# Kernel optimization log

Hardware: AMD Instinct MI355X
Metric: run time of the kernel (lower is better)

## Reference

```python
import jax, jax.numpy as jnp
from jax import lax
import numpy as np

EPS_BN = 1e-5


def _bn(x, g, b, axis):
    # eval-mode BatchNorm with running_mean=0, running_var=1
    shape = [1] * x.ndim
    shape[axis] = -1
    scale = (g / jnp.sqrt(1.0 + EPS_BN)).reshape(shape)
    return x * scale + b.reshape(shape)


def farthest_point_sample(xyz, npoint):
    B, N, _ = xyz.shape
    bidx = jnp.arange(B)

    def body(carry, _):
        dist, far = carry                      # [B,N], [B]
        centroid = xyz[bidx, far]              # [B,3]
        d = jnp.sum((xyz - centroid[:, None, :]) ** 2, axis=-1)
        dist = jnp.minimum(dist, d)
        return (dist, jnp.argmax(dist, axis=-1)), far

    init = (jnp.full((B, N), 1e10, xyz.dtype), jnp.zeros((B,), jnp.int32))
    _, idxs = lax.scan(body, init, None, length=npoint)
    return idxs.T                              # [B,npoint]


def square_distance(src, dst):
    # [B,S,3] x [B,N,3] -> [B,S,N]
    d = -2.0 * jnp.einsum('bsc,bnc->bsn', src, dst)
    d = d + jnp.sum(src ** 2, -1)[:, :, None] + jnp.sum(dst ** 2, -1)[:, None, :]
    return d


def sample_and_group(npoint, nsample, xyz, points):
    B = xyz.shape[0]
    bidx = jnp.arange(B)
    fps_idx = farthest_point_sample(xyz, npoint)          # [B,S]
    new_xyz = xyz[bidx[:, None], fps_idx]                 # [B,S,3]
    new_points = points[bidx[:, None], fps_idx]           # [B,S,C]
    dists = square_distance(new_xyz, xyz)                 # [B,S,N]
    _, idx = lax.top_k(-dists, nsample)                   # nearest nsample
    grouped = points[bidx[:, None, None], idx]            # [B,S,K,C]
    grouped_norm = grouped - new_points[:, :, None, :]
    rep = jnp.broadcast_to(new_points[:, :, None, :], grouped.shape)
    return new_xyz, jnp.concatenate([grouped_norm, rep], axis=-1)  # [B,S,K,2C]


def local_op(x, w, g, b):
    # x [B,S,K,D]; conv1d k=1 over channels D, BN, ReLU, max over K -> [B,out,S]
    y = jnp.einsum('bskd,od->bsko', x, w)
    y = jax.nn.relu(_bn(y, g, b, axis=3))
    y = jnp.max(y, axis=2)                                # [B,S,out]
    return jnp.transpose(y, (0, 2, 1))                    # [B,out,S]


def sa_layer(x, qk_w, v_w, v_b, t_w, t_b, g, b):
    # x [B,C,N]; q and k share weights (offset attention)
    xq = jnp.einsum('bcn,oc->bno', x, qk_w)               # [B,N,C/4]
    xk = jnp.einsum('bcn,oc->bon', x, qk_w)               # [B,C/4,N]
    xv = jnp.einsum('bcn,oc->bon', x, v_w) + v_b[:, None]
    energy = jnp.einsum('bnd,bdm->bnm', xq, xk)           # [B,N,N]
    attn = jax.nn.softmax(energy, axis=-1)
    attn = attn / (1e-9 + attn.sum(axis=1, keepdims=True))
    x_r = jnp.einsum('bcn,bnm->bcm', xv, attn)
    x_r = jnp.einsum('bcn,oc->bon', x - x_r, t_w) + t_b[:, None]
    x_r = jax.nn.relu(_bn(x_r, g, b, axis=1))
    return x + x_r


def setup_inputs() -> dict:
    key = jax.random.key(0)
    ks = iter(jax.random.split(key, 48))
    rn = lambda shape, s=0.05: jax.random.normal(next(ks), shape, jnp.float32) * s
    inp = {
        'xyz': jax.random.normal(next(ks), (32, 16384, 3), jnp.float32),
        'f': jax.random.normal(next(ks), (32, 16384, 3), jnp.float32),
        'conv1_w': rn((64, 6)), 'bn1_g': jnp.ones(64), 'bn1_b': jnp.zeros(64),
        'l0_w': rn((64, 128)), 'l0_g': jnp.ones(64), 'l0_b': jnp.zeros(64),
        'l1_w': rn((64, 128)), 'l1_g': jnp.ones(64), 'l1_b': jnp.zeros(64),
        'st_c1_w': rn((64, 64)), 'st_bn1_g': jnp.ones(64), 'st_bn1_b': jnp.zeros(64),
        'st_c2_w': rn((64, 64)), 'st_bn2_g': jnp.ones(64), 'st_bn2_b': jnp.zeros(64),
        'sa1_qk_w': rn((16, 64)), 'sa1_v_w': rn((64, 64)), 'sa1_v_b': jnp.zeros(64),
        'sa1_t_w': rn((64, 64)), 'sa1_t_b': jnp.zeros(64), 'sa1_g': jnp.ones(64), 'sa1_b': jnp.zeros(64),
        'sa2_qk_w': rn((16, 64)), 'sa2_v_w': rn((64, 64)), 'sa2_v_b': jnp.zeros(64),
        'sa2_t_w': rn((64, 64)), 'sa2_t_b': jnp.zeros(64), 'sa2_g': jnp.ones(64), 'sa2_b': jnp.zeros(64),
        'fuse_w': rn((256, 192)), 'fuse_g': jnp.ones(256), 'fuse_b': jnp.zeros(256),
        'lin1_w': rn((256, 256)), 'bn6_g': jnp.ones(256), 'bn6_b': jnp.zeros(256),
        'lin2_w': rn((256, 256)), 'lin2_b': jnp.zeros(256),
    }
    return inp


def _forward(xyz, f, conv1_w, bn1_g, bn1_b, l0_w, l0_g, l0_b, l1_w, l1_g, l1_b,
             st_c1_w, st_bn1_g, st_bn1_b, st_c2_w, st_bn2_g, st_bn2_b,
             sa1_qk_w, sa1_v_w, sa1_v_b, sa1_t_w, sa1_t_b, sa1_g, sa1_b,
             sa2_qk_w, sa2_v_w, sa2_v_b, sa2_t_w, sa2_t_b, sa2_g, sa2_b,
             fuse_w, fuse_g, fuse_b, lin1_w, bn6_g, bn6_b, lin2_w, lin2_b):
    center = jnp.mean(xyz, axis=1)                        # [B,3]
    xyz_c = xyz - center[:, None, :]
    pts = jnp.concatenate([xyz_c, f], axis=2)             # [B,N,6]
    geo = pts[..., :3]
    xin = jnp.transpose(pts, (0, 2, 1))                   # [B,6,N]
    x = jax.nn.relu(_bn(jnp.einsum('bcn,oc->bon', xin, conv1_w), bn1_g, bn1_b, 1))
    x = jnp.transpose(x, (0, 2, 1))                       # [B,N,64]
    new_xyz, nf = sample_and_group(128, 32, geo, x)
    feature_0 = local_op(nf, l0_w, l0_g, l0_b)            # [B,64,128]
    feature = jnp.transpose(feature_0, (0, 2, 1))
    _, nf2 = sample_and_group(32, 16, new_xyz, feature)
    feature_1 = local_op(nf2, l1_w, l1_g, l1_b)           # [B,64,32]
    # StackedAttention
    x = jax.nn.relu(_bn(jnp.einsum('bcn,oc->bon', feature_1, st_c1_w), st_bn1_g, st_bn1_b, 1))
    x = jax.nn.relu(_bn(jnp.einsum('bcn,oc->bon', x, st_c2_w), st_bn2_g, st_bn2_b, 1))
    x1 = sa_layer(x, sa1_qk_w, sa1_v_w, sa1_v_b, sa1_t_w, sa1_t_b, sa1_g, sa1_b)
    x2 = sa_layer(x1, sa2_qk_w, sa2_v_w, sa2_v_b, sa2_t_w, sa2_t_b, sa2_g, sa2_b)
    x = jnp.concatenate([x1, x2], axis=1)                 # [B,128,32]
    x = jnp.concatenate([x, feature_1], axis=1)           # [B,192,32]
    x = jax.nn.leaky_relu(_bn(jnp.einsum('bcn,oc->bon', x, fuse_w), fuse_g, fuse_b, 1), 0.2)
    x = jnp.max(x, axis=2)                                # [B,256]
    x = jax.nn.relu(_bn(x @ lin1_w.T, bn6_g, bn6_b, 1))   # dropout = identity (eval)
    x = x @ lin2_w.T + lin2_b
    return center, x


def reference(xyz, f, conv1_w, bn1_g, bn1_b, l0_w, l0_g, l0_b, l1_w, l1_g, l1_b,
              st_c1_w, st_bn1_g, st_bn1_b, st_c2_w, st_bn2_g, st_bn2_b,
              sa1_qk_w, sa1_v_w, sa1_v_b, sa1_t_w, sa1_t_b, sa1_g, sa1_b,
              sa2_qk_w, sa2_v_w, sa2_v_b, sa2_t_w, sa2_t_b, sa2_g, sa2_b,
              fuse_w, fuse_g, fuse_b, lin1_w, bn6_g, bn6_b, lin2_w, lin2_b):
    return _forward(xyz, f, conv1_w, bn1_g, bn1_b, l0_w, l0_g, l0_b, l1_w, l1_g, l1_b,
                    st_c1_w, st_bn1_g, st_bn1_b, st_c2_w, st_bn2_g, st_bn2_b,
                    sa1_qk_w, sa1_v_w, sa1_v_b, sa1_t_w, sa1_t_b, sa1_g, sa1_b,
                    sa2_qk_w, sa2_v_w, sa2_v_b, sa2_t_w, sa2_t_b, sa2_g, sa2_b,
                    fuse_w, fuse_g, fuse_b, lin1_w, bn6_g, bn6_b, lin2_w, lin2_b)
```

## Files before the change

kernel.cpp:

```cpp
#include <hip/hip_runtime.h>


__device__ __forceinline__ float bnscale(float g){ return g / sqrtf(1.0f + 1e-5f); }

__device__ __forceinline__ float conv_feat6(float p0,float p1,float p2,float p3,float p4,float p5,
                                            float w0,float w1,float w2,float w3,float w4,float w5,
                                            float sc,float bs){
    float y = p0*w0;
    y = fmaf(p1,w1,y); y = fmaf(p2,w2,y); y = fmaf(p3,w3,y);
    y = fmaf(p4,w4,y); y = fmaf(p5,w5,y);
    return fmaxf(fmaf(y,sc,bs), 0.0f);
}

__device__ __forceinline__ float fpsdist(float dx,float dy,float dz){
    #pragma clang fp contract(off)
    return (dx*dx + dy*dy) + dz*dz;
}

__device__ __forceinline__ float sumsq3(float x,float y,float z){
    #pragma clang fp contract(off)
    return (x*x + y*y) + z*z;
}
__device__ __forceinline__ float sqdist3(float qx,float qy,float qz,float qs,
                                         float px,float py,float pz){
    #pragma clang fp contract(off)
    {
        float dot = (qx*px + qy*py) + qz*pz;
        float pn  = (px*px + py*py) + pz*pz;
        return (-2.0f*dot + qs) + pn;
    }
}

__device__ __forceinline__ unsigned long long packdi(float d, unsigned int idx){
    unsigned int u = __float_as_uint(d);
    unsigned int msk = (unsigned int)((int)u >> 31);
    u ^= (msk | 0x80000000u);
    return ((unsigned long long)u << 32) | (unsigned long long)idx;
}

__device__ __forceinline__ unsigned long long u64min(unsigned long long a, unsigned long long b){
    return a < b ? a : b;
}

__device__ __forceinline__ unsigned long long u64_shfl_down(unsigned long long v, int off){
    unsigned int lo = (unsigned int)v, hi = (unsigned int)(v >> 32);
    lo = __shfl_down(lo, off, 64);
    hi = __shfl_down(hi, off, 64);
    return ((unsigned long long)hi << 32) | (unsigned long long)lo;
}

__device__ __forceinline__ unsigned long long u64_bcast0(unsigned long long v){
    unsigned int lo = (unsigned int)v, hi = (unsigned int)(v >> 32);
    lo = __shfl(lo, 0, 64);
    hi = __shfl(hi, 0, 64);
    return ((unsigned long long)hi << 32) | (unsigned long long)lo;
}

__global__ __launch_bounds__(1024, 1) void k_fps1(const float* __restrict__ xyz,
                                                  float* __restrict__ center,
                                                  float* __restrict__ out,
                                                  int* __restrict__ idx_out){
    constexpr int NTH = 1024, PPT = 16, N = 16384, NPOINT = 128, NW = 16;
    int b = blockIdx.x, t = threadIdx.x;
    int wid = t>>6, lane = t&63;

    __shared__ float s_red[NW][3];
    __shared__ unsigned int s_khi[2][NW], s_klo[2][NW];

    const float* xb = xyz + (size_t)b*N*3;
    float px[PPT], py[PPT], pz[PPT], dist[PPT];
    #pragma unroll
    for (int i=0;i<PPT;i++){
        const float* sp = xb + (size_t)(t + i*NTH)*3;
        px[i]=sp[0]; py[i]=sp[1]; pz[i]=sp[2];
        dist[i]=1e10f;
    }
    float sx=0.f, sy=0.f, sz=0.f;
    #pragma unroll
    for (int i=0;i<PPT;i++){ sx+=px[i]; sy+=py[i]; sz+=pz[i]; }
    #pragma unroll
    for (int off=32; off>=1; off>>=1){
        sx += __shfl_down(sx, off, 64);
        sy += __shfl_down(sy, off, 64);
        sz += __shfl_down(sz, off, 64);
    }
    if (lane==0){ s_red[wid][0]=sx; s_red[wid][1]=sy; s_red[wid][2]=sz; }
    __syncthreads();
    float cx0=0.f, cy0=0.f, cz0=0.f;
    #pragma unroll
    for (int w2=0; w2<NW; ++w2){ cx0+=s_red[w2][0]; cy0+=s_red[w2][1]; cz0+=s_red[w2][2]; }
    cx0 *= (1.0f/16384.0f); cy0 *= (1.0f/16384.0f); cz0 *= (1.0f/16384.0f);
    if (t < 3){
        float c = (t==0)?cx0:((t==1)?cy0:cz0);
        center[b*3+t] = c;
        out[b*3+t] = c;
    }
    #pragma unroll
    for (int i=0;i<PPT;i++){ px[i]-=cx0; py[i]-=cy0; pz[i]-=cz0; }
    if (t==0) idx_out[b*NPOINT] = 0;

    float cx = xb[0]-cx0, cy = xb[1]-cy0, cz = xb[2]-cz0;

    for (int it=1; it<NPOINT; ++it){
        int par = it & 1;
        float bv = -1.0f; int bis = 0;
        #pragma unroll
        for (int i=0;i<PPT;i++){
            float d = fpsdist(px[i]-cx, py[i]-cy, pz[i]-cz);
            float nd = fminf(dist[i], d);
            dist[i] = nd;
            bool better = nd > bv;
            bv  = better ? nd : bv;
            bis = better ? i  : bis;
        }
        int bi = t + (bis<<10);
        unsigned long long key = ((unsigned long long)__float_as_uint(bv) << 32)
                               | (unsigned long long)(unsigned)(~(unsigned)bi);
        #pragma unroll
        for (int off=32; off>=1; off>>=1){
            unsigned long long ok = u64_shfl_down(key, off);
            key = ok > key ? ok : key;
        }
        if (lane==0){ s_khi[par][wid]=(unsigned)(key>>32); s_klo[par][wid]=(unsigned)key; }
        __syncthreads();
        unsigned long long gk = ((unsigned long long)s_khi[par][0] << 32) | s_klo[par][0];
        #pragma unroll
        for (int w2=1; w2<NW; ++w2){
            unsigned long long k2 = ((unsigned long long)s_khi[par][w2] << 32) | s_klo[par][w2];
            if (k2 > gk) gk = k2;
        }
        int gi = (int)(~(unsigned)(gk & 0xFFFFFFFFull));
        gi = __builtin_amdgcn_readfirstlane(gi);
        if (t==0) idx_out[b*NPOINT + it] = gi;
        const float* wp = xb + (size_t)gi*3;
        cx = wp[0]-cx0; cy = wp[1]-cy0; cz = wp[2]-cz0;
    }
}

__global__ __launch_bounds__(256) void k_knn1(const float* __restrict__ xyz,
                                              const float* __restrict__ f,
                                              const float* __restrict__ center,
                                              const float* __restrict__ conv1_w,
                                              const float* __restrict__ bn1_g,
                                              const float* __restrict__ bn1_b,
                                              const int* __restrict__ fps_idx,
                                              float* __restrict__ new_xyz,
                                              float* __restrict__ np_feat,
                                              int* __restrict__ knn_idx){
    int t = threadIdx.x, wid = t>>6, lane = t&63;
    int q = blockIdx.x*4 + wid;
    int b = q>>7, s = q&127;

    float cx = center[b*3+0], cy = center[b*3+1], cz = center[b*3+2];
    int idx = fps_idx[b*128+s];
    const float* xp = xyz + ((size_t)b*16384 + idx)*3;
    const float* fp = f   + ((size_t)b*16384 + idx)*3;
    float p0 = xp[0]-cx, p1 = xp[1]-cy, p2 = xp[2]-cz;
    float p3 = fp[0], p4 = fp[1], p5 = fp[2];

    {
        const float* w6 = conv1_w + lane*6;
        float v = conv_feat6(p0,p1,p2,p3,p4,p5, w6[0],w6[1],w6[2],w6[3],w6[4],w6[5],
                             bnscale(bn1_g[lane]), bn1_b[lane]);
        np_feat[(size_t)q*64 + lane] = v;
        if (lane < 3){
            float pc = (lane==0)?p0:((lane==1)?p1:p2);
            new_xyz[(size_t)q*3 + lane] = pc;
        }
    }

    float qx = p0, qy = p1, qz = p2;
    float qs = sumsq3(qx,qy,qz);
    const float* xb = xyz + (size_t)b*16384*3;

    unsigned long long m0=~0ull, m1=~0ull, m2=~0ull, m3=~0ull;
    for (int i=0; i<256; i+=4){
        #pragma unroll
        for (int j=0;j<4;j++){
            int n = lane + ((i+j)<<6);
            const float* p = xb + (size_t)n*3;
            float dx = p[0]-cx, dy = p[1]-cy, dz = p[2]-cz;
            float d = sqdist3(qx,qy,qz,qs,dx,dy,dz);
            unsigned long long pk = packdi(d,(unsigned)n);
            if (j==0) m0 = u64min(m0,pk);
            else if (j==1) m1 = u64min(m1,pk);
            else if (j==2) m2 = u64min(m2,pk);
            else m3 = u64min(m3,pk);
        }
    }

    size_t kbase = (size_t)q*32;
    for (int r=0; r<32; ++r){
        unsigned long long mm = u64min(u64min(m0,m1), u64min(m2,m3));
        #pragma unroll
        for (int off=32; off>=1; off>>=1) mm = u64min(mm, u64_shfl_down(mm, off));
        unsigned long long win = u64_bcast0(mm);
        unsigned int widx = (unsigned int)(win & 0xFFFFFFFFull);
        if (lane==0) knn_idx[kbase + r] = (int)widx;
        int c = (int)(widx & 255u);
        int n2 = c + (lane<<8);
        const float* p = xb + (size_t)n2*3;
        float dx = p[0]-cx, dy = p[1]-cy, dz = p[2]-cz;
        float d = sqdist3(qx,qy,qz,qs,dx,dy,dz);
        unsigned long long pk = packdi(d,(unsigned)n2);
        if (pk <= win) pk = ~0ull;
        #pragma unroll
        for (int off=32; off>=1; off>>=1) pk = u64min(pk, u64_shfl_down(pk, off));
        unsigned long long nm = u64_bcast0(pk);
        int owner = c & 63, slot = c >> 6;
        if (lane == owner){
            if (slot==0) m0 = nm;
            else if (slot==1) m1 = nm;
            else if (slot==2) m2 = nm;
            else m3 = nm;
        }
    }
}

template<int K, int NQ, int NSRC, bool RECOMP>
__global__ __launch_bounds__(256, 2) void k_group_local(
    const float* __restrict__ xyz, const float* __restrict__ f, const float* __restrict__ center,
    const float* __restrict__ conv1_w, const float* __restrict__ bn1_g, const float* __restrict__ bn1_b,
    const float* __restrict__ src_feat,
    const int* __restrict__ knn_idx, const float* __restrict__ np_feat,
    const float* __restrict__ w, const float* __restrict__ g, const float* __restrict__ bb,
    float* __restrict__ out)
{
    __shared__ float wt[128*65];
    __shared__ float s_sc[64], s_bs[64];
    __shared__ float cwT[6*64];
    __shared__ float s_csc[64], s_cbs[64];
    __shared__ float np_l[4][64];
    __shared__ float gda[4][K][64];
    __shared__ float s_pts[4][K][6];

    int t = threadIdx.x;
    for (int e=t; e<8192; e+=256){ int o = e>>7, d = e&127; wt[d*65 + o] = w[e]; }
    if (t < 64){ s_sc[t] = bnscale(g[t]); s_bs[t] = bb[t]; }
    if constexpr (RECOMP){
        for (int e=t; e<384; e+=256){ int o = e/6, j = e%6; cwT[j*64 + o] = conv1_w[e]; }
        if (t < 64){ s_csc[t] = bnscale(bn1_g[t]); s_cbs[t] = bn1_b[t]; }
    }
    __syncthreads();

    int wid = t>>6, lane = t&63;
    int q = blockIdx.x*4 + wid;
    int b = q / NQ, s = q % NQ;

    float np_o = np_feat[((size_t)b*NQ + s)*64 + lane];
    np_l[wid][lane] = np_o;

    const int* kix = knn_idx + ((size_t)b*NQ + s)*K;

    if constexpr (RECOMP){
        float cx = center[b*3+0], cy = center[b*3+1], cz = center[b*3+2];
        if (lane < K){
            int myi = kix[lane];
            const float* xp = xyz + ((size_t)b*16384 + myi)*3;
            s_pts[wid][lane][0] = xp[0]-cx;
            s_pts[wid][lane][1] = xp[1]-cy;
            s_pts[wid][lane][2] = xp[2]-cz;
            const float* fp = f + ((size_t)b*16384 + myi)*3;
            s_pts[wid][lane][3] = fp[0];
            s_pts[wid][lane][4] = fp[1];
            s_pts[wid][lane][5] = fp[2];
        }
        #pragma unroll
        for (int k=0; k<K; ++k){
            float gv = conv_feat6(s_pts[wid][k][0], s_pts[wid][k][1], s_pts[wid][k][2],
                                  s_pts[wid][k][3], s_pts[wid][k][4], s_pts[wid][k][5],
                                  cwT[0*64+lane], cwT[1*64+lane], cwT[2*64+lane],
                                  cwT[3*64+lane], cwT[4*64+lane], cwT[5*64+lane],
                                  s_csc[lane], s_cbs[lane]);
            gda[wid][k][lane] = gv - np_o;
        }
    } else {
        int myi = kix[lane < K ? lane : 0];
        #pragma unroll
        for (int k=0; k<K; ++k){
            int ik = __shfl(myi, k, 64);
            gda[wid][k][lane] = src_feat[((size_t)b*NSRC + ik)*64 + lane] - np_o;
        }
    }

    float C = 0.f;
    #pragma unroll
    for (int d=0; d<64; d++) C = fmaf(np_l[wid][d], wt[(64+d)*65 + lane], C);

    float acc_y[K];
    #pragma unroll
    for (int k=0;k<K;k++) acc_y[k] = C;

    #pragma unroll
    for (int c=0; c<2; ++c){
        float wr[32];
        #pragma unroll
        for (int j=0;j<32;j++) wr[j] = wt[(c*32+j)*65 + lane];
        #pragma unroll
        for (int k=0;k<K;k++){
            const float4* g4 = (const float4*)&gda[wid][k][c*32];
            float yk = 0.f;
            #pragma unroll
            for (int j4=0;j4<8;j4++){
                float4 gg = g4[j4];
                yk = fmaf(gg.x, wr[j4*4+0], yk);
                yk = fmaf(gg.y, wr[j4*4+1], yk);
                yk = fmaf(gg.z, wr[j4*4+2], yk);
                yk = fmaf(gg.w, wr[j4*4+3], yk);
            }
            acc_y[k] = acc_y[k] + yk;
        }
    }

    float acc = -1e30f;
    #pragma unroll
    for (int k=0;k<K;k++){
        float v = fmaxf(fmaf(acc_y[k], s_sc[lane], s_bs[lane]), 0.0f);
        acc = fmaxf(acc, v);
    }
    out[((size_t)b*NQ + s)*64 + lane] = acc;
}

__device__ void sa_block(const float* X, float* Xout,
                         float* Q, float* E, float* XV, float* XR, float* CS,
                         const float* qk_w, const float* v_w, const float* v_b,
                         const float* t_w, const float* t_b,
                         const float* g, const float* bb, int t)
{
    constexpr int NT = 1024;
    for (int e=t; e<512; e+=NT){
        int n = e>>4, o = e&15;
        float y = 0.f;
        for (int c=0;c<64;c++) y = fmaf(qk_w[o*64+c], X[c*32+n], y);
        Q[n*16+o] = y;
    }
    for (int e=t; e<2048; e+=NT){
        int o = e>>5, n = e&31;
        float y = v_b[o];
        for (int c=0;c<64;c++) y = fmaf(v_w[o*64+c], X[c*32+n], y);
        XV[o*32+n] = y;
    }
    __syncthreads();
    {
        int n = t>>5, m = t&31;
        float y = 0.f;
        for (int d=0;d<16;d++) y = fmaf(Q[n*16+d], Q[m*16+d], y);
        E[t] = y;
    }
    __syncthreads();
    {
        float v = E[t];
        float mx = v;
        #pragma unroll
        for (int mk=16; mk>=1; mk>>=1) mx = fmaxf(mx, __shfl_xor(mx, mk, 64));
        float p = expf(v - mx);
        float sum = p;
        #pragma unroll
        for (int mk=16; mk>=1; mk>>=1) sum += __shfl_xor(sum, mk, 64);
        E[t] = p / sum;
    }
    __syncthreads();
    if (t < 32){
        float cs = 0.f;
        for (int n=0;n<32;n++) cs += E[n*32+t];
        CS[t] = 1e-9f + cs;
    }
    __syncthreads();
    E[t] = E[t] / CS[t&31];
    __syncthreads();
    for (int e=t; e<2048; e+=NT){
        int c = e>>5, m = e&31;
        float y = 0.f;
        for (int n=0;n<32;n++) y = fmaf(XV[c*32+n], E[n*32+m], y);
        XR[c*32+m] = y;
    }
    __syncthreads();
    for (int e=t; e<2048; e+=NT){
        int o = e>>5, n = e&31;
        float y = 0.f;
        for (int c=0;c<64;c++) y = fmaf(t_w[o*64+c], X[c*32+n]-XR[c*32+n], y);
        y += t_b[o];
        y = fmaxf(fmaf(y, bnscale(g[o]), bb[o]), 0.0f);
        Xout[e] = X[e] + y;
    }
    __syncthreads();
}

__global__ __launch_bounds__(1024) void k_mega(
    const float* __restrict__ new_xyz1,
    const float* __restrict__ feat,
    const float* __restrict__ l1_w, const float* __restrict__ l1_g, const float* __restrict__ l1_b,
    const float* st_c1_w, const float* st_bn1_g, const float* st_bn1_b,
    const float* st_c2_w, const float* st_bn2_g, const float* st_bn2_b,
    const float* sa1_qk, const float* sa1_v, const float* sa1_vb,
    const float* sa1_t, const float* sa1_tb, const float* sa1_g, const float* sa1_b,
    const float* sa2_qk, const float* sa2_v, const float* sa2_vb,
    const float* sa2_t, const float* sa2_tb, const float* sa2_g, const float* sa2_b,
    const float* fuse_w, const float* fuse_g, const float* fuse_b,
    const float* lin1_w, const float* bn6_g, const float* bn6_b,
    const float* lin2_w, const float* lin2_b,
    float* __restrict__ out)
{
    constexpr int NT = 1024;
    __shared__ float nx1[384];
    __shared__ int   s_i2[32];
    __shared__ float np2L[2048];
    __shared__ float nx2[96];
    __shared__ int   s_k2[512];
    __shared__ float wt[8320];
    __shared__ float s_sc[64], s_bs[64];
    __shared__ float smt[15168];

    int b = blockIdx.x, t = threadIdx.x, wid = t>>6, lane = t&63;

    for (int e=t; e<384; e+=NT) nx1[e] = new_xyz1[(size_t)b*384 + e];
    for (int e=t; e<8192; e+=NT){ int o = e>>7, d = e&127; wt[d*65 + o] = l1_w[e]; }
    if (t < 64){ s_sc[t] = bnscale(l1_g[t]); s_bs[t] = l1_b[t]; }
    __syncthreads();

    if (wid == 0){
        float px[2],py[2],pz[2],dist[2];
        #pragma unroll
        for (int i=0;i<2;i++){
            int n = lane + i*64;
            px[i]=nx1[n*3+0]; py[i]=nx1[n*3+1]; pz[i]=nx1[n*3+2];
            dist[i]=1e10f;
        }
        if (lane==0) s_i2[0] = 0;
        float cx=nx1[0], cy=nx1[1], cz=nx1[2];
        for (int it=1; it<32; ++it){
            float bv=-1.0f; int bi=0;
            float bx=0.f, by=0.f, bz=0.f;
            #pragma unroll
            for (int i=0;i<2;i++){
                float d = fpsdist(px[i]-cx, py[i]-cy, pz[i]-cz);
                float nd = fminf(dist[i], d);
                dist[i]=nd;
                bool better = nd > bv;
                bv = better ? nd : bv;
                bi = better ? (lane + i*64) : bi;
                bx = better ? px[i] : bx;
                by = better ? py[i] : by;
                bz = better ? pz[i] : bz;
            }
            unsigned long long key = ((unsigned long long)__float_as_uint(bv) << 32)
                                   | (unsigned long long)(unsigned)(~(unsigned)bi);
            #pragma unroll
            for (int off=32; off>=1; off>>=1){
                unsigned long long ok = u64_shfl_down(key, off);
                float ox = __shfl_down(bx, off, 64);
                float oy = __shfl_down(by, off, 64);
                float oz = __shfl_down(bz, off, 64);
                bool better = ok > key;
                key = better ? ok : key;
                bx = better ? ox : bx;
                by = better ? oy : by;
                bz = better ? oz : bz;
            }
            key = u64_bcast0(key);
            cx = __shfl(bx, 0, 64); cy = __shfl(by, 0, 64); cz = __shfl(bz, 0, 64);
            if (lane==0) s_i2[it] = (int)(~(unsigned)(key & 0xFFFFFFFFull));
        }
    }
    __syncthreads();

    for (int e=t; e<2048; e+=NT){
        int s = e>>6, o = e&63;
        np2L[s*64 + o] = feat[((size_t)b*128 + s_i2[s])*64 + o];
    }
    if (t < 32){
        int idx = s_i2[t];
        nx2[t*3+0] = nx1[idx*3+0];
        nx2[t*3+1] = nx1[idx*3+1];
        nx2[t*3+2] = nx1[idx*3+2];
    }
    __syncthreads();

    for (int j=0;j<2;j++){
        int s = wid + 16*j;
        float qx = nx2[s*3+0], qy = nx2[s*3+1], qz = nx2[s*3+2];
        float qs = sumsq3(qx,qy,qz);
        unsigned long long pp0, pp1;
        {
            float ax=nx1[lane*3+0], ay=nx1[lane*3+1], az=nx1[lane*3+2];
            pp0 = packdi(sqdist3(qx,qy,qz,qs,ax,ay,az), (unsigned)lane);
            ax=nx1[(lane+64)*3+0]; ay=nx1[(lane+64)*3+1]; az=nx1[(lane+64)*3+2];
            pp1 = packdi(sqdist3(qx,qy,qz,qs,ax,ay,az), (unsigned)(lane+64));
        }
        for (int r=0; r<16; ++r){
            unsigned long long mm = u64min(pp0, pp1);
            #pragma unroll
            for (int off=32; off>=1; off>>=1) mm = u64min(mm, u64_shfl_down(mm, off));
            unsigned long long win = u64_bcast0(mm);
            if (lane==0) s_k2[s*16 + r] = (int)(win & 0xFFFFFFFFull);
            if (pp0 == win) pp0 = ~0ull;
            if (pp1 == win) pp1 = ~0ull;
        }
    }
    __syncthreads();

    float* gda = smt + 2112;
    for (int j=0;j<2;j++){
        int s = wid + 16*j;
        float np_o = np2L[s*64 + lane];
        float C0 = 0.f;
        #pragma unroll
        for (int d=0; d<64; d++) C0 = fmaf(np2L[s*64 + d], wt[(64+d)*65 + lane], C0);
        float acc_y[16];
        #pragma unroll
        for (int k=0;k<16;k++) acc_y[k] = C0;
        #pragma unroll
        for (int half=0; half<2; ++half){
            #pragma unroll
            for (int kk=0;kk<8;++kk){
                int ik = s_k2[s*16 + half*8 + kk];
                gda[(wid*8+kk)*64 + lane] = feat[((size_t)b*128 + ik)*64 + lane] - np_o;
            }
            #pragma unroll
            for (int c=0; c<2; ++c){
                float wr[32];
                #pragma unroll
                for (int jj=0;jj<32;jj++) wr[jj] = wt[(c*32+jj)*65 + lane];
                #pragma unroll
                for (int kk=0;kk<8;++kk){
                    const float4* g4 = (const float4*)&gda[(wid*8+kk)*64 + c*32];
                    float yk = 0.f;
                    #pragma unroll
                    for (int j4=0;j4<8;j4++){
                        float4 gg = g4[j4];
                        yk = fmaf(gg.x, wr[j4*4+0], yk);
                        yk = fmaf(gg.y, wr[j4*4+1], yk);
                        yk = fmaf(gg.z, wr[j4*4+2], yk);
                        yk = fmaf(gg.w, wr[j4*4+3], yk);
                    }
                    acc_y[half*8+kk] = acc_y[half*8+kk] + yk;
                }
            }
        }
        float acc = -1e30f;
        #pragma unroll
        for (int k=0;k<16;k++){
            float v = fmaxf(fmaf(acc_y[k], s_sc[lane], s_bs[lane]), 0.0f);
            acc = fmaxf(acc, v);
        }
        smt[lane*33 + s] = acc;
    }
    __syncthreads();

    float* F1 = smt;
    float* XA = smt + 2112;
    float* XB = smt + 4160;
    float* Q  = smt + 6208;
    float* E  = smt + 6720;
    float* XV = smt + 7744;
    float* XR = smt + 9792;
    float* CS = smt + 11840;
    float* FO = smt + 6208;
    float* PO = smt + 14656;
    float* P2 = smt + 14912;

    for (int e=t; e<2048; e+=NT){
        int o = e>>5, n = e&31;
        float y = 0.f;
        for (int c=0;c<64;c++) y = fmaf(st_c1_w[o*64+c], F1[c*33+n], y);
        XA[e] = fmaxf(fmaf(y, bnscale(st_bn1_g[o]), st_bn1_b[o]), 0.0f);
    }
    __syncthreads();
    for (int e=t; e<2048; e+=NT){
        int o = e>>5, n = e&31;
        float y = 0.f;
        for (int c=0;c<64;c++) y = fmaf(st_c2_w[o*64+c], XA[c*32+n], y);
        XB[e] = fmaxf(fmaf(y, bnscale(st_bn2_g[o]), st_bn2_b[o]), 0.0f);
    }
    __syncthreads();
    sa_block(XB, XA, Q,E,XV,XR,CS, sa1_qk, sa1_v, sa1_vb, sa1_t, sa1_tb, sa1_g, sa1_b, t);
    sa_block(XA, XB, Q,E,XV,XR,CS, sa2_qk, sa2_v, sa2_vb, sa2_t, sa2_tb, sa2_g, sa2_b, t);
    for (int e=t; e<8192; e+=NT){
        int o = e>>5, n = e&31;
        const float* wr = fuse_w + o*192;
        float y = 0.f;
        for (int c=0;c<64;c++) y = fmaf(wr[c],      XA[c*32+n], y);
        for (int c=0;c<64;c++) y = fmaf(wr[64+c],   XB[c*32+n], y);
        for (int c=0;c<64;c++) y = fmaf(wr[128+c],  F1[c*33+n], y);
        float v = fmaf(y, bnscale(fuse_g[o]), fuse_b[o]);
        FO[o*33+n] = (v > 0.0f) ? v : 0.2f*v;
    }
    __syncthreads();
    if (t < 256){
        float mx = -1e30f;
        for (int n=0;n<32;n++) mx = fmaxf(mx, FO[t*33+n]);
        PO[t] = mx;
    }
    __syncthreads();
    if (t < 256){
        const float* wr = lin1_w + t*256;
        float y = 0.f;
        for (int c=0;c<256;c++) y = fmaf(wr[c], PO[c], y);
        P2[t] = fmaxf(fmaf(y, bnscale(bn6_g[t]), bn6_b[t]), 0.0f);
    }
    __syncthreads();
    if (t < 256){
        const float* wr = lin2_w + t*256;
        float y = 0.f;
        for (int c=0;c<256;c++) y = fmaf(wr[c], P2[c], y);
        out[96 + b*256 + t] = y + lin2_b[t];
    }
}

extern "C" void kernel_launch(void* const* d_in, const int* in_sizes, int n_in,
                              void* d_out, int out_size, void* d_ws, size_t ws_size,
                              hipStream_t stream)
{
    const float* xyz      = (const float*)d_in[0];
    const float* f        = (const float*)d_in[1];
    const float* conv1_w  = (const float*)d_in[2];
    const float* bn1_g    = (const float*)d_in[3];
    const float* bn1_b    = (const float*)d_in[4];
    const float* l0_w     = (const float*)d_in[5];
    const float* l0_g     = (const float*)d_in[6];
    const float* l0_b     = (const float*)d_in[7];
    const float* l1_w     = (const float*)d_in[8];
    const float* l1_g     = (const float*)d_in[9];
    const float* l1_b     = (const float*)d_in[10];
    const float* st_c1_w  = (const float*)d_in[11];
    const float* st_bn1_g = (const float*)d_in[12];
    const float* st_bn1_b = (const float*)d_in[13];
    const float* st_c2_w  = (const float*)d_in[14];
    const float* st_bn2_g = (const float*)d_in[15];
    const float* st_bn2_b = (const float*)d_in[16];
    const float* sa1_qk   = (const float*)d_in[17];
    const float* sa1_v    = (const float*)d_in[18];
    const float* sa1_vb   = (const float*)d_in[19];
    const float* sa1_t    = (const float*)d_in[20];
    const float* sa1_tb   = (const float*)d_in[21];
    const float* sa1_g    = (const float*)d_in[22];
    const float* sa1_b    = (const float*)d_in[23];
    const float* sa2_qk   = (const float*)d_in[24];
    const float* sa2_v    = (const float*)d_in[25];
    const float* sa2_vb   = (const float*)d_in[26];
    const float* sa2_t    = (const float*)d_in[27];
    const float* sa2_tb   = (const float*)d_in[28];
    const float* sa2_g    = (const float*)d_in[29];
    const float* sa2_b    = (const float*)d_in[30];
    const float* fuse_w   = (const float*)d_in[31];
    const float* fuse_g   = (const float*)d_in[32];
    const float* fuse_b   = (const float*)d_in[33];
    const float* lin1_w   = (const float*)d_in[34];
    const float* bn6_g    = (const float*)d_in[35];
    const float* bn6_b    = (const float*)d_in[36];
    const float* lin2_w   = (const float*)d_in[37];
    const float* lin2_b   = (const float*)d_in[38];
    float* out = (float*)d_out;

    float* ws = (float*)d_ws;
    float* center   = ws + 0;
    float* new_xyz1 = ws + 96;
    float* np1      = ws + 12384;
    float* feat     = ws + 274528;
    int*   fps1     = (int*)(ws + 536672);
    int*   knn1     = (int*)(ws + 540768);

    k_fps1<<<32, 1024, 0, stream>>>(xyz, center, out, fps1);
    k_knn1<<<1024, 256, 0, stream>>>(xyz, f, center, conv1_w, bn1_g, bn1_b,
                                     fps1, new_xyz1, np1, knn1);
    k_group_local<32,128,1,true><<<1024, 256, 0, stream>>>(
        xyz, f, center, conv1_w, bn1_g, bn1_b, nullptr, knn1, np1, l0_w, l0_g, l0_b, feat);
    k_mega<<<32, 1024, 0, stream>>>(new_xyz1, feat,
        l1_w, l1_g, l1_b,
        st_c1_w, st_bn1_g, st_bn1_b, st_c2_w, st_bn2_g, st_bn2_b,
        sa1_qk, sa1_v, sa1_vb, sa1_t, sa1_tb, sa1_g, sa1_b,
        sa2_qk, sa2_v, sa2_vb, sa2_t, sa2_tb, sa2_g, sa2_b,
        fuse_w, fuse_g, fuse_b, lin1_w, bn6_g, bn6_b, lin2_w, lin2_b, out);
}
```

Measured before the change: 724.3 us.

## Precompute centered float4 xyz with norms; stream FPS points from memory, halve block size

FPS now writes centered xyz plus squared norm as a float4 array to workspace. Each FPS iteration re-reads its points from that array instead of holding them in registers, and the block shrinks to 512 threads with 32 points per thread. The kNN and grouping kernels read the precomputed float4 points and norms, which removes the center subtraction and norm recompute, and the mega kernel is resized to 512 threads. The intent is vectorized loads and shared preprocessing, at the cost of FPS re-reading global or cache memory on every one of its 128 iterations with half the thread parallelism.

```diff
diff --git a/kernel.cpp b/kernel.cpp
--- a/kernel.cpp
+++ b/kernel.cpp
@@ -30,6 +30,14 @@
         return (-2.0f*dot + qs) + pn;
     }
 }
+__device__ __forceinline__ float sqdist3_pn(float qx,float qy,float qz,float qs,
+                                            float px,float py,float pz,float pn){
+    #pragma clang fp contract(off)
+    {
+        float dot = (qx*px + qy*py) + qz*pz;
+        return (-2.0f*dot + qs) + pn;
+    }
+}
 
 __device__ __forceinline__ unsigned long long packdi(float d, unsigned int idx){
     unsigned int u = __float_as_uint(d);
@@ -56,11 +64,11 @@
     return ((unsigned long long)hi << 32) | (unsigned long long)lo;
 }
 
-__global__ __launch_bounds__(1024, 1) void k_fps1(const float* __restrict__ xyz,
-                                                  float* __restrict__ center,
-                                                  float* __restrict__ out,
-                                                  int* __restrict__ idx_out){
-    constexpr int NTH = 1024, PPT = 16, N = 16384, NPOINT = 128, NW = 16;
+__global__ __launch_bounds__(512, 1) void k_fps1(const float* __restrict__ xyz,
+                                                 float4* xyzc,
+                                                 float* __restrict__ out,
+                                                 int* __restrict__ idx_out){
+    constexpr int NTH = 512, PPT = 32, N = 16384, NPOINT = 128, NW = 8;
     int b = blockIdx.x, t = threadIdx.x;
     int wid = t>>6, lane = t&63;
 
@@ -68,16 +76,13 @@
     __shared__ unsigned int s_khi[2][NW], s_klo[2][NW];
 
     const float* xb = xyz + (size_t)b*N*3;
-    float px[PPT], py[PPT], pz[PPT], dist[PPT];
-    #pragma unroll
+    float4* xc = xyzc + (size_t)b*N;
+
+    float sx=0.f, sy=0.f, sz=0.f;
     for (int i=0;i<PPT;i++){
         const float* sp = xb + (size_t)(t + i*NTH)*3;
-        px[i]=sp[0]; py[i]=sp[1]; pz[i]=sp[2];
-        dist[i]=1e10f;
-    }
-    float sx=0.f, sy=0.f, sz=0.f;
-    #pragma unroll
-    for (int i=0;i<PPT;i++){ sx+=px[i]; sy+=py[i]; sz+=pz[i]; }
+        sx += sp[0]; sy += sp[1]; sz += sp[2];
+    }
     #pragma unroll
     for (int off=32; off>=1; off>>=1){
         sx += __shfl_down(sx, off, 64);
@@ -92,28 +97,39 @@
     cx0 *= (1.0f/16384.0f); cy0 *= (1.0f/16384.0f); cz0 *= (1.0f/16384.0f);
     if (t < 3){
         float c = (t==0)?cx0:((t==1)?cy0:cz0);
-        center[b*3+t] = c;
         out[b*3+t] = c;
     }
-    #pragma unroll
-    for (int i=0;i<PPT;i++){ px[i]-=cx0; py[i]-=cy0; pz[i]-=cz0; }
+
+    for (int i=0;i<PPT;i++){
+        int n = t + i*NTH;
+        const float* sp = xb + (size_t)n*3;
+        float ax = sp[0]-cx0, ay = sp[1]-cy0, az = sp[2]-cz0;
+        xc[n] = make_float4(ax, ay, az, sumsq3(ax,ay,az));
+    }
     if (t==0) idx_out[b*NPOINT] = 0;
 
+    float dist[PPT];
+    #pragma unroll
+    for (int i=0;i<PPT;i++) dist[i]=1e10f;
+
     float cx = xb[0]-cx0, cy = xb[1]-cy0, cz = xb[2]-cz0;
+    __syncthreads();
 
     for (int it=1; it<NPOINT; ++it){
+        asm volatile("" ::: "memory");
         int par = it & 1;
         float bv = -1.0f; int bis = 0;
         #pragma unroll
         for (int i=0;i<PPT;i++){
-            float d = fpsdist(px[i]-cx, py[i]-cy, pz[i]-cz);
+            float4 p = xc[t + i*NTH];
+            float d = fpsdist(p.x-cx, p.y-cy, p.z-cz);
             float nd = fminf(dist[i], d);
             dist[i] = nd;
             bool better = nd > bv;
             bv  = better ? nd : bv;
             bis = better ? i  : bis;
         }
-        int bi = t + (bis<<10);
+        int bi = t + (bis<<9);
         unsigned long long key = ((unsigned long long)__float_as_uint(bv) << 32)
                                | (unsigned long long)(unsigned)(~(unsigned)bi);
         #pragma unroll
@@ -137,9 +153,8 @@
     }
 }
 
-__global__ __launch_bounds__(256) void k_knn1(const float* __restrict__ xyz,
+__global__ __launch_bounds__(256) void k_knn1(const float4* __restrict__ xyzc,
                                               const float* __restrict__ f,
-                                              const float* __restrict__ center,
                                               const float* __restrict__ conv1_w,
                                               const float* __restrict__ bn1_g,
                                               const float* __restrict__ bn1_b,
@@ -151,11 +166,11 @@
     int q = blockIdx.x*4 + wid;
     int b = q>>7, s = q&127;
 
-    float cx = center[b*3+0], cy = center[b*3+1], cz = center[b*3+2];
     int idx = fps_idx[b*128+s];
-    const float* xp = xyz + ((size_t)b*16384 + idx)*3;
-    const float* fp = f   + ((size_t)b*16384 + idx)*3;
-    float p0 = xp[0]-cx, p1 = xp[1]-cy, p2 = xp[2]-cz;
+    const float4* xcb = xyzc + (size_t)b*16384;
+    float4 qc = xcb[idx];
+    float p0 = qc.x, p1 = qc.y, p2 = qc.z;
+    const float* fp = f + ((size_t)b*16384 + idx)*3;
     float p3 = fp[0], p4 = fp[1], p5 = fp[2];
 
     {
@@ -170,17 +185,15 @@
     }
 
     float qx = p0, qy = p1, qz = p2;
-    float qs = sumsq3(qx,qy,qz);
-    const float* xb = xyz + (size_t)b*16384*3;
+    float qs = qc.w;
 
     unsigned long long m0=~0ull, m1=~0ull, m2=~0ull, m3=~0ull;
     for (int i=0; i<256; i+=4){
         #pragma unroll
         for (int j=0;j<4;j++){
             int n = lane + ((i+j)<<6);
-            const float* p = xb + (size_t)n*3;
-            float dx = p[0]-cx, dy = p[1]-cy, dz = p[2]-cz;
-            float d = sqdist3(qx,qy,qz,qs,dx,dy,dz);
+            float4 pc = xcb[n];
+            float d = sqdist3_pn(qx,qy,qz,qs, pc.x,pc.y,pc.z, pc.w);
             unsigned long long pk = packdi(d,(unsigned)n);
             if (j==0) m0 = u64min(m0,pk);
             else if (j==1) m1 = u64min(m1,pk);
@@ -199,9 +212,8 @@
         if (lane==0) knn_idx[kbase + r] = (int)widx;
         int c = (int)(widx & 255u);
         int n2 = c + (lane<<8);
-        const float* p = xb + (size_t)n2*3;
-        float dx = p[0]-cx, dy = p[1]-cy, dz = p[2]-cz;
-        float d = sqdist3(qx,qy,qz,qs,dx,dy,dz);
+        float4 pc = xcb[n2];
+        float d = sqdist3_pn(qx,qy,qz,qs, pc.x,pc.y,pc.z, pc.w);
         unsigned long long pk = packdi(d,(unsigned)n2);
         if (pk <= win) pk = ~0ull;
         #pragma unroll
@@ -217,11 +229,10 @@
     }
 }
 
-template<int K, int NQ, int NSRC, bool RECOMP>
+template<int K, int NQ>
 __global__ __launch_bounds__(256, 2) void k_group_local(
-    const float* __restrict__ xyz, const float* __restrict__ f, const float* __restrict__ center,
+    const float4* __restrict__ xyzc, const float* __restrict__ f,
     const float* __restrict__ conv1_w, const float* __restrict__ bn1_g, const float* __restrict__ bn1_b,
-    const float* __restrict__ src_feat,
     const int* __restrict__ knn_idx, const float* __restrict__ np_feat,
     const float* __restrict__ w, const float* __restrict__ g, const float* __restrict__ bb,
     float* __restrict__ out)
@@ -237,10 +248,8 @@
     int t = threadIdx.x;
     for (int e=t; e<8192; e+=256){ int o = e>>7, d = e&127; wt[d*65 + o] = w[e]; }
     if (t < 64){ s_sc[t] = bnscale(g[t]); s_bs[t] = bb[t]; }
-    if constexpr (RECOMP){
-        for (int e=t; e<384; e+=256){ int o = e/6, j = e%6; cwT[j*64 + o] = conv1_w[e]; }
-        if (t < 64){ s_csc[t] = bnscale(bn1_g[t]); s_cbs[t] = bn1_b[t]; }
-    }
+    for (int e=t; e<384; e+=256){ int o = e/6, j = e%6; cwT[j*64 + o] = conv1_w[e]; }
+    if (t < 64){ s_csc[t] = bnscale(bn1_g[t]); s_cbs[t] = bn1_b[t]; }
     __syncthreads();
 
     int wid = t>>6, lane = t&63;
@@ -252,35 +261,25 @@
 
     const int* kix = knn_idx + ((size_t)b*NQ + s)*K;
 
-    if constexpr (RECOMP){
-        float cx = center[b*3+0], cy = center[b*3+1], cz = center[b*3+2];
-        if (lane < K){
-            int myi = kix[lane];
-            const float* xp = xyz + ((size_t)b*16384 + myi)*3;
-            s_pts[wid][lane][0] = xp[0]-cx;
-            s_pts[wid][lane][1] = xp[1]-cy;
-            s_pts[wid][lane][2] = xp[2]-cz;
-            const float* fp = f + ((size_t)b*16384 + myi)*3;
-            s_pts[wid][lane][3] = fp[0];
-            s_pts[wid][lane][4] = fp[1];
-            s_pts[wid][lane][5] = fp[2];
-        }
-        #pragma unroll
-        for (int k=0; k<K; ++k){
-            float gv = conv_feat6(s_pts[wid][k][0], s_pts[wid][k][1], s_pts[wid][k][2],
-                                  s_pts[wid][k][3], s_pts[wid][k][4], s_pts[wid][k][5],
-                                  cwT[0*64+lane], cwT[1*64+lane], cwT[2*64+lane],
-                                  cwT[3*64+lane], cwT[4*64+lane], cwT[5*64+lane],
-                                  s_csc[lane], s_cbs[lane]);
-            gda[wid][k][lane] = gv - np_o;
-        }
-    } else {
-        int myi = kix[lane < K ? lane : 0];
-        #pragma unroll
-        for (int k=0; k<K; ++k){
-            int ik = __shfl(myi, k, 64);
-            gda[wid][k][lane] = src_feat[((size_t)b*NSRC + ik)*64 + lane] - np_o;
-        }
+    if (lane < K){
+        int myi = kix[lane];
+        float4 pc = xyzc[(size_t)b*16384 + myi];
+        s_pts[wid][lane][0] = pc.x;
+        s_pts[wid][lane][1] = pc.y;
+        s_pts[wid][lane][2] = pc.z;
+        const float* fp = f + ((size_t)b*16384 + myi)*3;
+        s_pts[wid][lane][3] = fp[0];
+        s_pts[wid][lane][4] = fp[1];
+        s_pts[wid][lane][5] = fp[2];
+    }
+    #pragma unroll
+    for (int k=0; k<K; ++k){
+        float gv = conv_feat6(s_pts[wid][k][0], s_pts[wid][k][1], s_pts[wid][k][2],
+                              s_pts[wid][k][3], s_pts[wid][k][4], s_pts[wid][k][5],
+                              cwT[0*64+lane], cwT[1*64+lane], cwT[2*64+lane],
+                              cwT[3*64+lane], cwT[4*64+lane], cwT[5*64+lane],
+                              s_csc[lane], s_cbs[lane]);
+        gda[wid][k][lane] = gv - np_o;
     }
 
     float C = 0.f;
@@ -327,7 +326,7 @@
                          const float* t_w, const float* t_b,
                          const float* g, const float* bb, int t)
 {
-    constexpr int NT = 1024;
+    constexpr int NT = 512;
     for (int e=t; e<512; e+=NT){
         int n = e>>4, o = e&15;
         float y = 0.f;
@@ -341,15 +340,15 @@
         XV[o*32+n] = y;
     }
     __syncthreads();
-    {
-        int n = t>>5, m = t&31;
+    for (int e=t; e<1024; e+=NT){
+        int n = e>>5, m = e&31;
         float y = 0.f;
         for (int d=0;d<16;d++) y = fmaf(Q[n*16+d], Q[m*16+d], y);
-        E[t] = y;
-    }
-    __syncthreads();
-    {
-        float v = E[t];
+        E[e] = y;
+    }
+    __syncthreads();
+    for (int e=t; e<1024; e+=NT){
+        float v = E[e];
         float mx = v;
         #pragma unroll
         for (int mk=16; mk>=1; mk>>=1) mx = fmaxf(mx, __shfl_xor(mx, mk, 64));
@@ -357,7 +356,7 @@
         float sum = p;
         #pragma unroll
         for (int mk=16; mk>=1; mk>>=1) sum += __shfl_xor(sum, mk, 64);
-        E[t] = p / sum;
+        E[e] = p / sum;
     }
     __syncthreads();
     if (t < 32){
@@ -366,7 +365,7 @@
         CS[t] = 1e-9f + cs;
     }
     __syncthreads();
-    E[t] = E[t] / CS[t&31];
+    for (int e=t; e<1024; e+=NT) E[e] = E[e] / CS[e&31];
     __syncthreads();
     for (int e=t; e<2048; e+=NT){
         int c = e>>5, m = e&31;
@@ -386,7 +385,7 @@
     __syncthreads();
 }
 
-__global__ __launch_bounds__(1024) void k_mega(
+__global__ __launch_bounds__(512, 1) void k_mega(
     const float* __restrict__ new_xyz1,
     const float* __restrict__ feat,
     const float* __restrict__ l1_w, const float* __restrict__ l1_g, const float* __restrict__ l1_b,
@@ -401,7 +400,7 @@
     const float* lin2_w, const float* lin2_b,
     float* __restrict__ out)
 {
-    constexpr int NT = 1024;
+    constexpr int NT = 512;
     __shared__ float nx1[384];
     __shared__ int   s_i2[32];
     __shared__ float np2L[2048];
@@ -476,8 +475,8 @@
     }
     __syncthreads();
 
-    for (int j=0;j<2;j++){
-        int s = wid + 16*j;
+    for (int j=0;j<4;j++){
+        int s = wid + 8*j;
         float qx = nx2[s*3+0], qy = nx2[s*3+1], qz = nx2[s*3+2];
         float qs = sumsq3(qx,qy,qz);
         unsigned long long pp0, pp1;
@@ -500,8 +499,8 @@
     __syncthreads();
 
     float* gda = smt + 2112;
-    for (int j=0;j<2;j++){
-        int s = wid + 16*j;
+    for (int j=0;j<4;j++){
+        int s = wid + 8*j;
         float np_o = np2L[s*64 + lane];
         float C0 = 0.f;
         #pragma unroll
@@ -653,19 +652,19 @@
     float* out = (float*)d_out;
 
     float* ws = (float*)d_ws;
-    float* center   = ws + 0;
-    float* new_xyz1 = ws + 96;
-    float* np1      = ws + 12384;
-    float* feat     = ws + 274528;
-    int*   fps1     = (int*)(ws + 536672);
-    int*   knn1     = (int*)(ws + 540768);
-
-    k_fps1<<<32, 1024, 0, stream>>>(xyz, center, out, fps1);
-    k_knn1<<<1024, 256, 0, stream>>>(xyz, f, center, conv1_w, bn1_g, bn1_b,
+    float4* xyzc    = (float4*)ws;
+    float* new_xyz1 = ws + 2097152;
+    float* np1      = ws + 2109440;
+    float* feat     = ws + 2371584;
+    int*   fps1     = (int*)(ws + 2633728);
+    int*   knn1     = (int*)(ws + 2637824);
+
+    k_fps1<<<32, 512, 0, stream>>>(xyz, xyzc, out, fps1);
+    k_knn1<<<1024, 256, 0, stream>>>(xyzc, f, conv1_w, bn1_g, bn1_b,
                                      fps1, new_xyz1, np1, knn1);
-    k_group_local<32,128,1,true><<<1024, 256, 0, stream>>>(
-        xyz, f, center, conv1_w, bn1_g, bn1_b, nullptr, knn1, np1, l0_w, l0_g, l0_b, feat);
-    k_mega<<<32, 1024, 0, stream>>>(new_xyz1, feat,
+    k_group_local<32,128><<<1024, 256, 0, stream>>>(
+        xyzc, f, conv1_w, bn1_g, bn1_b, knn1, np1, l0_w, l0_g, l0_b, feat);
+    k_mega<<<32, 512, 0, stream>>>(new_xyz1, feat,
         l1_w, l1_g, l1_b,
         st_c1_w, st_bn1_g, st_bn1_b, st_c2_w, st_bn2_g, st_bn2_b,
         sa1_qk, sa1_v, sa1_vb, sa1_t, sa1_tb, sa1_g, sa1_b,
```

Measured after the change: 827.2 us. 14.2% more time.
